# Kernel tuning notes

Measured on AMD Instinct MI355X. Metric: run time of the kernel, lower is better.

The kernel has to match this reference:

```python
import jax, jax.numpy as jnp
import numpy as np

D = 128
N_AUTHOR = 100000
N_PAPER = 200000
N_LAYERS = 2


def setup_inputs() -> dict:
    key = jax.random.key(0)
    ks = jax.random.split(key, 16)
    inp = {
        "x_author": jax.random.normal(ks[0], (N_AUTHOR, D), dtype=jnp.float32),
        "x_paper": jax.random.normal(ks[1], (N_PAPER, D), dtype=jnp.float32),
        "edge_index": jax.random.randint(ks[2], (2, 500000), 0, 100000, dtype=jnp.int32),
        "coauthor_edge_index": jax.random.randint(ks[3], (2, 250000), 0, 100000, dtype=jnp.int32),
        "supervision_edge_index": jax.random.randint(ks[4], (2, 100000), 0, 100000, dtype=jnp.int32),
    }
    scale = 1.0 / np.sqrt(D)
    names = ["W_a2p", "W_p2a", "W_aself", "W_pself", "W_co"]
    for i, n in enumerate(names):
        inp[n] = jax.random.uniform(ks[5 + i], (N_LAYERS, D, D), jnp.float32, -scale, scale)
        inp["b" + n[1:]] = jax.random.uniform(ks[10 + i], (N_LAYERS, D), jnp.float32, -scale, scale)
    return inp


def _linear(x, W, b):
    # torch.nn.Linear: y = x @ W.T + b
    return x @ W.T + b


def reference(x_author, x_paper, edge_index, coauthor_edge_index, supervision_edge_index,
              W_a2p, b_a2p, W_p2a, b_p2a, W_aself, b_aself, W_pself, b_pself, W_co, b_co):
    author_idx, paper_idx = edge_index[0], edge_index[1]
    co_src, co_dst = coauthor_edge_index[0], coauthor_edge_index[1]
    for l in range(N_LAYERS):
        # author -> paper messages
        msg_a = _linear(x_author[author_idx], W_a2p[l], b_a2p[l])       # [E, D]
        agg_to_papers = jax.ops.segment_sum(msg_a, paper_idx, num_segments=x_paper.shape[0])
        # paper -> author messages
        msg_p = _linear(x_paper[paper_idx], W_p2a[l], b_p2a[l])         # [E, D]
        agg_to_authors = jax.ops.segment_sum(msg_p, author_idx, num_segments=x_author.shape[0])
        x_paper = agg_to_papers + _linear(x_paper, W_pself[l], b_pself[l])
        x_author = agg_to_authors + _linear(x_author, W_aself[l], b_aself[l])
        # coauthor edges (author -> author)
        msg_co = _linear(x_author[co_src], W_co[l], b_co[l])            # [E_co, D]
        agg_co = jax.ops.segment_sum(msg_co, co_dst, num_segments=x_author.shape[0])
        x_author = x_author + agg_co
    a = x_author[supervision_edge_index[0]]
    p = x_paper[supervision_edge_index[1]]
    return (a * p).sum(axis=1)
```

## Files before the change

### kernel.cpp

```cpp
#include <hip/hip_runtime.h>

#define DD 128

typedef __attribute__((ext_vector_type(8))) short short8;
typedef __attribute__((ext_vector_type(4))) float f32x4;

__device__ inline unsigned short f2bf(float f) {
    unsigned u = __float_as_uint(f);
    unsigned r = (u + 0x7fffu + ((u >> 16) & 1u)) >> 16;
    return (unsigned short)r;
}
__device__ inline float bf2f(unsigned short u) {
    return __uint_as_float(((unsigned)u) << 16);
}
__device__ inline float bflo(unsigned u) { return __uint_as_float(u << 16); }
__device__ inline float bfhi(unsigned u) { return __uint_as_float(u & 0xffff0000u); }
__device__ inline unsigned pack2(float a, float b) {
    return (unsigned)f2bf(a) | ((unsigned)f2bf(b) << 16);
}

__global__ __launch_bounds__(256) void conv_all(const float* __restrict__ inA, unsigned short* __restrict__ outA, int n4A,
                                                const float* __restrict__ inP, unsigned short* __restrict__ outP, int n4P) {
    int i = blockIdx.x * blockDim.x + threadIdx.x;
    const float* in;
    unsigned short* out;
    int j;
    if (i < n4A) { in = inA; out = outA; j = i; }
    else if (i < n4A + n4P) { in = inP; out = outP; j = i - n4A; }
    else return;
    float4 v = *(const float4*)(in + (size_t)j * 4);
    uint2 o;
    o.x = pack2(v.x, v.y);
    o.y = pack2(v.z, v.w);
    *(uint2*)(out + (size_t)j * 4) = o;
}

__global__ __launch_bounds__(256) void pack_all(const float* __restrict__ Wa2p, const float* __restrict__ Wpself,
                                                const float* __restrict__ Wp2a, const float* __restrict__ Waself,
                                                const float* __restrict__ Wco,
                                                short* __restrict__ BPp0, short* __restrict__ BPp1,
                                                short* __restrict__ BPa0, short* __restrict__ BPa1,
                                                short* __restrict__ BPc0, short* __restrict__ BPc1) {
    const int WL = 128 * 128;
    int idx = blockIdx.x * blockDim.x + threadIdx.x;
    int seg = idx >> 12;
    int sidx = idx & 4095;
    const float *W1, *W2;
    short* dst;
    int ktiles;
    switch (seg) {
        case 0: W1 = Wa2p;      W2 = Wpself;      dst = BPp0; ktiles = 8; break;
        case 1: W1 = Wa2p + WL; W2 = Wpself + WL; dst = BPp1; ktiles = 8; break;
        case 2: W1 = Wp2a;      W2 = Waself;      dst = BPa0; ktiles = 8; break;
        case 3: W1 = Wp2a + WL; W2 = Waself + WL; dst = BPa1; ktiles = 8; break;
        case 4: W1 = Wco;       W2 = nullptr;     dst = BPc0; ktiles = 4; break;
        default: W1 = Wco + WL; W2 = nullptr;     dst = BPc1; ktiles = 4; break;
    }
    int total = 8 * ktiles * 64;
    if (sidx >= total) return;
    int lane = sidx & 63;
    int kk = (sidx >> 6) % ktiles;
    int t = (sidx >> 6) / ktiles;
    int n = t * 16 + (lane & 15);
    int kbase = kk * 32 + (lane >> 4) * 8;
    short8 v;
#pragma unroll
    for (int j = 0; j < 8; ++j) {
        int k = kbase + j;
        float f = (k < 128) ? W1[n * 128 + k] : W2[n * 128 + (k - 128)];
        v[j] = (short)f2bf(f);
    }
    *(short8*)(dst + (size_t)sidx * 8) = v;
}

__global__ __launch_bounds__(256) void count_all(const int* __restrict__ aidx, const int* __restrict__ pidx,
                                                 const int* __restrict__ cod,
                                                 int* __restrict__ cntP, int* __restrict__ cntA,
                                                 int* __restrict__ cntC, int E, int Eco) {
    int i = blockIdx.x * blockDim.x + threadIdx.x;
    if (i < E) {
        atomicAdd(&cntP[pidx[i]], 1);
        atomicAdd(&cntA[aidx[i]], 1);
    } else if (i < E + Eco) {
        atomicAdd(&cntC[cod[i - E]], 1);
    }
}

__global__ __launch_bounds__(256) void scan_local3(const int* __restrict__ c0, int* __restrict__ r0, int* __restrict__ p0, int N0,
                                                   const int* __restrict__ c1, int* __restrict__ r1, int* __restrict__ p1, int N1,
                                                   const int* __restrict__ c2, int* __restrict__ r2, int* __restrict__ p2, int N2,
                                                   int nb0, int nb1) {
    __shared__ int sh[256];
    int b = blockIdx.x;
    const int* cnt; int* row; int* partials; int N; int lb;
    if (b < nb0) { cnt = c0; row = r0; partials = p0; N = N0; lb = b; }
    else if (b < nb0 + nb1) { cnt = c1; row = r1; partials = p1; N = N1; lb = b - nb0; }
    else { cnt = c2; row = r2; partials = p2; N = N2; lb = b - nb0 - nb1; }
    int t = threadIdx.x;
    int base = lb * 1024 + t * 4;
    int v0 = 0, v1 = 0, v2 = 0, v3 = 0;
    if (base + 0 < N) v0 = cnt[base + 0];
    if (base + 1 < N) v1 = cnt[base + 1];
    if (base + 2 < N) v2 = cnt[base + 2];
    if (base + 3 < N) v3 = cnt[base + 3];
    sh[t] = v0 + v1 + v2 + v3;
    __syncthreads();
    for (int off = 1; off < 256; off <<= 1) {
        int y = (t >= off) ? sh[t - off] : 0;
        __syncthreads();
        sh[t] += y;
        __syncthreads();
    }
    int excl = (t > 0) ? sh[t - 1] : 0;
    if (t == 255) partials[lb] = sh[255];
    if (base + 0 < N) row[base + 0] = excl; excl += v0;
    if (base + 1 < N) row[base + 1] = excl; excl += v1;
    if (base + 2 < N) row[base + 2] = excl; excl += v2;
    if (base + 3 < N) row[base + 3] = excl;
}

__global__ __launch_bounds__(256) void scan_partials3(int* __restrict__ p0, int nb0,
                                                      int* __restrict__ p1, int nb1,
                                                      int* __restrict__ p2, int nb2) {
    __shared__ int sh[256];
    int* partials; int nb;
    if (blockIdx.x == 0) { partials = p0; nb = nb0; }
    else if (blockIdx.x == 1) { partials = p1; nb = nb1; }
    else { partials = p2; nb = nb2; }
    int t = threadIdx.x;
    int v = (t < nb) ? partials[t] : 0;
    sh[t] = v;
    __syncthreads();
    for (int off = 1; off < 256; off <<= 1) {
        int y = (t >= off) ? sh[t - off] : 0;
        __syncthreads();
        sh[t] += y;
        __syncthreads();
    }
    if (t < nb) partials[t] = (t > 0) ? sh[t - 1] : 0;
}

__global__ __launch_bounds__(256) void scan_finalize3(int* __restrict__ r0, int* __restrict__ cu0, const int* __restrict__ p0, int N0,
                                                      int* __restrict__ r1, int* __restrict__ cu1, const int* __restrict__ p1, int N1,
                                                      int* __restrict__ r2, int* __restrict__ cu2, const int* __restrict__ p2, int N2,
                                                      int fb0, int fb1) {
    int b = blockIdx.x;
    int* row; int* cur; const int* partials; int N; int lb;
    if (b < fb0) { row = r0; cur = cu0; partials = p0; N = N0; lb = b; }
    else if (b < fb0 + fb1) { row = r1; cur = cu1; partials = p1; N = N1; lb = b - fb0; }
    else { row = r2; cur = cu2; partials = p2; N = N2; lb = b - fb0 - fb1; }
    int i = lb * 256 + threadIdx.x;
    if (i >= N) return;
    int r = row[i] + partials[i >> 10];
    row[i] = r;
    cur[i] = r;
}

__global__ __launch_bounds__(256) void fill_all(const int* __restrict__ aidx, const int* __restrict__ pidx,
                                                const int* __restrict__ cos_, const int* __restrict__ cod,
                                                int* __restrict__ curP, int* __restrict__ curA, int* __restrict__ curC,
                                                int* __restrict__ adjP, int* __restrict__ adjA, int* __restrict__ adjC,
                                                int E, int Eco) {
    int i = blockIdx.x * blockDim.x + threadIdx.x;
    if (i < E) {
        int a = aidx[i], pp = pidx[i];
        adjP[atomicAdd(&curP[pp], 1)] = a;
        adjA[atomicAdd(&curA[a], 1)] = pp;
    } else if (i < E + Eco) {
        adjC[atomicAdd(&curC[cod[i - E]], 1)] = cos_[i - E];
    }
}

struct FParams {
    const unsigned short* gsrc;
    const unsigned short* selfx;
    const unsigned short* base;
    const int* adj;
    const int* rowp;
    const int* cnt;
    const short* Bpack;
    const float* b1;
    const float* b2;
    unsigned short* out;
    int M;
};

template <int KTILES, bool HAS_B2, bool ADD_BASE>
__device__ __forceinline__ void fused_body(char* lds, const FParams& p, int blk) {
    const int tid = threadIdx.x;
    const int node0 = blk * 64;
    const int grp = tid >> 4;
    const int l = tid & 15;

    int stA[4], dA[4];
#pragma unroll
    for (int i = 0; i < 4; ++i) {
        int node = node0 + grp * 4 + i;
        bool ok = node < p.M;
        stA[i] = ok ? p.rowp[node] : 0;
        dA[i] = ok ? p.cnt[node] : 0;
    }

    float acc[4][8];
#pragma unroll
    for (int i = 0; i < 4; ++i)
#pragma unroll
        for (int j = 0; j < 8; ++j) acc[i][j] = 0.f;

    int dmax = dA[0];
#pragma unroll
    for (int i = 1; i < 4; ++i) dmax = dA[i] > dmax ? dA[i] : dmax;

    for (int k = 0; k < dmax; k += 4) {
#pragma unroll
        for (int i = 0; i < 4; ++i) {
            if (k < dA[i]) {
                int st = stA[i] + k;
                int rem = dA[i] - k;
                int s0 = p.adj[st];
                int s1 = p.adj[st + ((rem > 1) ? 1 : 0)];
                int s2 = p.adj[st + ((rem > 2) ? 2 : 0)];
                int s3 = p.adj[st + ((rem > 3) ? 3 : 0)];
                float w1 = (rem > 1) ? 1.f : 0.f;
                float w2 = (rem > 2) ? 1.f : 0.f;
                float w3 = (rem > 3) ? 1.f : 0.f;
                uint4 v0 = *(const uint4*)(p.gsrc + (size_t)s0 * DD + l * 8);
                uint4 v1 = *(const uint4*)(p.gsrc + (size_t)s1 * DD + l * 8);
                uint4 v2 = *(const uint4*)(p.gsrc + (size_t)s2 * DD + l * 8);
                uint4 v3 = *(const uint4*)(p.gsrc + (size_t)s3 * DD + l * 8);
                acc[i][0] += bflo(v0.x); acc[i][1] += bfhi(v0.x);
                acc[i][2] += bflo(v0.y); acc[i][3] += bfhi(v0.y);
                acc[i][4] += bflo(v0.z); acc[i][5] += bfhi(v0.z);
                acc[i][6] += bflo(v0.w); acc[i][7] += bfhi(v0.w);
                acc[i][0] += w1 * bflo(v1.x); acc[i][1] += w1 * bfhi(v1.x);
                acc[i][2] += w1 * bflo(v1.y); acc[i][3] += w1 * bfhi(v1.y);
                acc[i][4] += w1 * bflo(v1.z); acc[i][5] += w1 * bfhi(v1.z);
                acc[i][6] += w1 * bflo(v1.w); acc[i][7] += w1 * bfhi(v1.w);
                acc[i][0] += w2 * bflo(v2.x); acc[i][1] += w2 * bfhi(v2.x);
                acc[i][2] += w2 * bflo(v2.y); acc[i][3] += w2 * bfhi(v2.y);
                acc[i][4] += w2 * bflo(v2.z); acc[i][5] += w2 * bfhi(v2.z);
                acc[i][6] += w2 * bflo(v2.w); acc[i][7] += w2 * bfhi(v2.w);
                acc[i][0] += w3 * bflo(v3.x); acc[i][1] += w3 * bfhi(v3.x);
                acc[i][2] += w3 * bflo(v3.y); acc[i][3] += w3 * bfhi(v3.y);
                acc[i][4] += w3 * bflo(v3.z); acc[i][5] += w3 * bfhi(v3.z);
                acc[i][6] += w3 * bflo(v3.w); acc[i][7] += w3 * bfhi(v3.w);
            }
        }
    }

#pragma unroll
    for (int i = 0; i < 4; ++i) {
        int lr = grp * 4 + i;
        uint4 o = make_uint4(pack2(acc[i][0], acc[i][1]), pack2(acc[i][2], acc[i][3]),
                             pack2(acc[i][4], acc[i][5]), pack2(acc[i][6], acc[i][7]));
        int colb = l * 16;
        *(uint4*)(lds + lr * 256 + (colb ^ ((lr & 7) << 4))) = o;
    }
    __syncthreads();

    const int wave = tid >> 6;
    const int lane = tid & 63;
    const int kg = lane >> 4;
    const int lrA = wave * 16 + (lane & 15);

    f32x4 facc[8];
#pragma unroll
    for (int t = 0; t < 8; ++t) facc[t] = (f32x4){0.f, 0.f, 0.f, 0.f};

#pragma unroll
    for (int kk = 0; kk < 4; ++kk) {
        int colb = kk * 64 + kg * 16;
        short8 af = *(const short8*)(lds + lrA * 256 + (colb ^ ((lrA & 7) << 4)));
#pragma unroll
        for (int t = 0; t < 8; ++t) {
            short8 bf = *(const short8*)(p.Bpack + ((size_t)(t * KTILES + kk) * 64 + lane) * 8);
            facc[t] = __builtin_amdgcn_mfma_f32_16x16x32_bf16(af, bf, facc[t], 0, 0, 0);
        }
    }
    if (KTILES == 8) {
        int srow = node0 + wave * 16 + (lane & 15);
        if (srow >= p.M) srow = p.M - 1;
        const unsigned short* sp = p.selfx + (size_t)srow * DD + kg * 8;
#pragma unroll
        for (int kk = 4; kk < 8; ++kk) {
            short8 af = *(const short8*)(sp + (kk - 4) * 32);
#pragma unroll
            for (int t = 0; t < 8; ++t) {
                short8 bf = *(const short8*)(p.Bpack + ((size_t)(t * 8 + kk) * 64 + lane) * 8);
                facc[t] = __builtin_amdgcn_mfma_f32_16x16x32_bf16(af, bf, facc[t], 0, 0, 0);
            }
        }
    }

    const int col0 = lane & 15;
    const int crow0 = node0 + wave * 16 + kg * 4;
#pragma unroll
    for (int t = 0; t < 8; ++t) {
        int col = t * 16 + col0;
        float bb = p.b1[col];
        float b2v = HAS_B2 ? p.b2[col] : 0.f;
#pragma unroll
        for (int r = 0; r < 4; ++r) {
            int row = crow0 + r;
            if (row < p.M) {
                float v = facc[t][r] + (float)p.cnt[row] * bb + b2v;
                if (ADD_BASE) v += bf2f(p.base[(size_t)row * DD + col]);
                p.out[(size_t)row * DD + col] = f2bf(v);
            }
        }
    }
}

__global__ __launch_bounds__(256, 5) void fused_dual_kernel(FParams pP, FParams pA, int blkP) {
    __shared__ char lds[16384];
    bool isP = (int)blockIdx.x < blkP;
    const FParams& p = isP ? pP : pA;
    fused_body<8, true, false>(lds, p, isP ? blockIdx.x : blockIdx.x - blkP);
}

__global__ __launch_bounds__(256, 5) void fused_co_kernel(FParams p) {
    __shared__ char lds[16384];
    fused_body<4, false, true>(lds, p, blockIdx.x);
}

__global__ __launch_bounds__(256) void dot_kernel(
    const unsigned short* __restrict__ xa, const unsigned short* __restrict__ xp,
    const int* __restrict__ s0, const int* __restrict__ s1,
    float* __restrict__ out, int E) {
    int g = blockIdx.x * blockDim.x + threadIdx.x;
    int e = g >> 4;
    int l = g & 15;
    if (e >= E) return;
    int a = s0[e], p = s1[e];
    uint4 va = *(const uint4*)(xa + (size_t)a * DD + l * 8);
    uint4 vp = *(const uint4*)(xp + (size_t)p * DD + l * 8);
    float s = bflo(va.x) * bflo(vp.x) + bfhi(va.x) * bfhi(vp.x)
            + bflo(va.y) * bflo(vp.y) + bfhi(va.y) * bfhi(vp.y)
            + bflo(va.z) * bflo(vp.z) + bfhi(va.z) * bfhi(vp.z)
            + bflo(va.w) * bflo(vp.w) + bfhi(va.w) * bfhi(vp.w);
    s += __shfl_xor(s, 1); s += __shfl_xor(s, 2);
    s += __shfl_xor(s, 4); s += __shfl_xor(s, 8);
    if (l == 0) out[e] = s;
}

extern "C" void kernel_launch(void* const* d_in, const int* in_sizes, int n_in,
                              void* d_out, int out_size, void* d_ws, size_t ws_size,
                              hipStream_t stream) {
    const float* xa_in = (const float*)d_in[0];
    const float* xp_in = (const float*)d_in[1];
    const int* eidx = (const int*)d_in[2];
    const int* co = (const int*)d_in[3];
    const int* sup = (const int*)d_in[4];
    const float* W_a2p = (const float*)d_in[5];
    const float* b_a2p = (const float*)d_in[6];
    const float* W_p2a = (const float*)d_in[7];
    const float* b_p2a = (const float*)d_in[8];
    const float* W_aself = (const float*)d_in[9];
    const float* b_aself = (const float*)d_in[10];
    const float* W_pself = (const float*)d_in[11];
    const float* b_pself = (const float*)d_in[12];
    const float* W_co = (const float*)d_in[13];
    const float* b_co = (const float*)d_in[14];

    const int NA = in_sizes[0] / DD;
    const int NP = in_sizes[1] / DD;
    const int E = in_sizes[2] / 2;
    const int Eco = in_sizes[3] / 2;
    const int Esup = in_sizes[4] / 2;
    const int* a_idx = eidx;
    const int* p_idx = eidx + E;
    const int* co_s = co;
    const int* co_d = co + Eco;
    const int* s0 = sup;
    const int* s1 = sup + Esup;

    char* w = (char*)d_ws;
    auto carve = [&](size_t bytes) -> char* {
        char* p = w;
        w += (bytes + 255) & ~(size_t)255;
        return p;
    };
    unsigned short* XA = (unsigned short*)carve((size_t)NA * DD * 2);
    unsigned short* XP = (unsigned short*)carve((size_t)NP * DD * 2);
    unsigned short* P0b = (unsigned short*)carve((size_t)NP * DD * 2);
    unsigned short* P1b = (unsigned short*)carve((size_t)NP * DD * 2);
    unsigned short* A0b = (unsigned short*)carve((size_t)NA * DD * 2);
    unsigned short* A1b = (unsigned short*)carve((size_t)NA * DD * 2);
    int* cntP = (int*)carve((size_t)NP * 4);
    int* rowP = (int*)carve((size_t)NP * 4);
    int* curP = (int*)carve((size_t)NP * 4);
    int* cntA = (int*)carve((size_t)NA * 4);
    int* rowA = (int*)carve((size_t)NA * 4);
    int* curA = (int*)carve((size_t)NA * 4);
    int* cntC = (int*)carve((size_t)NA * 4);
    int* rowC = (int*)carve((size_t)NA * 4);
    int* curC = (int*)carve((size_t)NA * 4);
    int* adjP = (int*)carve((size_t)E * 4);
    int* adjA = (int*)carve((size_t)E * 4);
    int* adjC = (int*)carve((size_t)Eco * 4);
    int* partP = (int*)carve(256 * 4);
    int* partA = (int*)carve(256 * 4);
    int* partC = (int*)carve(256 * 4);
    short* BPp0 = (short*)carve(8 * 8 * 64 * 8 * 2);
    short* BPp1 = (short*)carve(8 * 8 * 64 * 8 * 2);
    short* BPa0 = (short*)carve(8 * 8 * 64 * 8 * 2);
    short* BPa1 = (short*)carve(8 * 8 * 64 * 8 * 2);
    short* BPc0 = (short*)carve(8 * 4 * 64 * 8 * 2);
    short* BPc1 = (short*)carve(8 * 4 * 64 * 8 * 2);

    int n4A = NA * DD / 4, n4P = NP * DD / 4;
    conv_all<<<(n4A + n4P + 255) / 256, 256, 0, stream>>>(xa_in, XA, n4A, xp_in, XP, n4P);
    pack_all<<<96, 256, 0, stream>>>(W_a2p, W_pself, W_p2a, W_aself, W_co, BPp0, BPp1, BPa0, BPa1, BPc0, BPc1);

    hipMemsetAsync(cntP, 0, (size_t)NP * 4, stream);
    hipMemsetAsync(cntA, 0, (size_t)NA * 4, stream);
    hipMemsetAsync(cntC, 0, (size_t)NA * 4, stream);
    count_all<<<(E + Eco + 255) / 256, 256, 0, stream>>>(a_idx, p_idx, co_d, cntP, cntA, cntC, E, Eco);
    const int nbP = (NP + 1023) / 1024;
    const int nbA = (NA + 1023) / 1024;
    scan_local3<<<nbP + nbA + nbA, 256, 0, stream>>>(cntP, rowP, partP, NP, cntA, rowA, partA, NA, cntC, rowC, partC, NA, nbP, nbA);
    scan_partials3<<<3, 256, 0, stream>>>(partP, nbP, partA, nbA, partC, nbA);
    const int fbP = (NP + 255) / 256;
    const int fbA = (NA + 255) / 256;
    scan_finalize3<<<fbP + fbA + fbA, 256, 0, stream>>>(rowP, curP, partP, NP, rowA, curA, partA, NA, rowC, curC, partC, NA, fbP, fbA);
    fill_all<<<(E + Eco + 255) / 256, 256, 0, stream>>>(a_idx, p_idx, co_s, co_d, curP, curA, curC, adjP, adjA, adjC, E, Eco);

    const int blkP = (NP + 63) / 64;
    const int blkA = (NA + 63) / 64;

    FParams pP1 = {XA, XP, nullptr, adjP, rowP, cntP, BPp0, b_a2p, b_pself, P0b, NP};
    FParams pA1 = {XP, XA, nullptr, adjA, rowA, cntA, BPa0, b_p2a, b_aself, A0b, NA};
    FParams pC1 = {A0b, nullptr, A0b, adjC, rowC, cntC, BPc0, b_co, nullptr, A1b, NA};
    FParams pP2 = {A1b, P0b, nullptr, adjP, rowP, cntP, BPp1, b_a2p + 128, b_pself + 128, P1b, NP};
    FParams pA2 = {P0b, A1b, nullptr, adjA, rowA, cntA, BPa1, b_p2a + 128, b_aself + 128, A0b, NA};
    FParams pC2 = {A0b, nullptr, A0b, adjC, rowC, cntC, BPc1, b_co + 128, nullptr, A1b, NA};

    fused_dual_kernel<<<blkP + blkA, 256, 0, stream>>>(pP1, pA1, blkP);
    fused_co_kernel<<<blkA, 256, 0, stream>>>(pC1);
    fused_dual_kernel<<<blkP + blkA, 256, 0, stream>>>(pP2, pA2, blkP);
    fused_co_kernel<<<blkA, 256, 0, stream>>>(pC2);

    dot_kernel<<<(Esup * 16 + 255) / 256, 256, 0, stream>>>(A1b, P1b, s0, s1, (float*)d_out, Esup);
}
```

Baseline: 536.9 us.

## Stage block adjacency in LDS, halve gather unroll, raise occupancy, merge memsets

```diff
diff --git a/kernel.cpp b/kernel.cpp
--- a/kernel.cpp
+++ b/kernel.cpp
@@ -1,6 +1,7 @@
 #include <hip/hip_runtime.h>
 
 #define DD 128
+#define ADJ_CAP 1024
 
 typedef __attribute__((ext_vector_type(8))) short short8;
 typedef __attribute__((ext_vector_type(4))) float f32x4;
@@ -186,20 +187,27 @@
 };
 
 template <int KTILES, bool HAS_B2, bool ADD_BASE>
-__device__ __forceinline__ void fused_body(char* lds, const FParams& p, int blk) {
+__device__ __forceinline__ void fused_body(char* lds, int* ldsAdj, const FParams& p, int blk) {
     const int tid = threadIdx.x;
     const int node0 = blk * 64;
     const int grp = tid >> 4;
     const int l = tid & 15;
 
-    int stA[4], dA[4];
+    const int lastNode = (node0 + 63 < p.M) ? node0 + 63 : p.M - 1;
+    const int est = p.rowp[node0];
+    const int eend = p.rowp[lastNode] + p.cnt[lastNode];
+    const int nE = eend - est;
+    for (int j = tid; j < nE && j < ADJ_CAP; j += 256) ldsAdj[j] = p.adj[est + j];
+
+    int relSt[4], dA[4];
 #pragma unroll
     for (int i = 0; i < 4; ++i) {
         int node = node0 + grp * 4 + i;
         bool ok = node < p.M;
-        stA[i] = ok ? p.rowp[node] : 0;
+        relSt[i] = ok ? (p.rowp[node] - est) : 0;
         dA[i] = ok ? p.cnt[node] : 0;
     }
+    __syncthreads();
 
     float acc[4][8];
 #pragma unroll
@@ -211,23 +219,18 @@
 #pragma unroll
     for (int i = 1; i < 4; ++i) dmax = dA[i] > dmax ? dA[i] : dmax;
 
-    for (int k = 0; k < dmax; k += 4) {
+    for (int k = 0; k < dmax; k += 2) {
 #pragma unroll
         for (int i = 0; i < 4; ++i) {
             if (k < dA[i]) {
-                int st = stA[i] + k;
                 int rem = dA[i] - k;
-                int s0 = p.adj[st];
-                int s1 = p.adj[st + ((rem > 1) ? 1 : 0)];
-                int s2 = p.adj[st + ((rem > 2) ? 2 : 0)];
-                int s3 = p.adj[st + ((rem > 3) ? 3 : 0)];
+                int o0 = relSt[i] + k;
+                int o1 = o0 + ((rem > 1) ? 1 : 0);
+                int s0 = (o0 < ADJ_CAP) ? ldsAdj[o0] : p.adj[est + o0];
+                int s1 = (o1 < ADJ_CAP) ? ldsAdj[o1] : p.adj[est + o1];
                 float w1 = (rem > 1) ? 1.f : 0.f;
-                float w2 = (rem > 2) ? 1.f : 0.f;
-                float w3 = (rem > 3) ? 1.f : 0.f;
                 uint4 v0 = *(const uint4*)(p.gsrc + (size_t)s0 * DD + l * 8);
                 uint4 v1 = *(const uint4*)(p.gsrc + (size_t)s1 * DD + l * 8);
-                uint4 v2 = *(const uint4*)(p.gsrc + (size_t)s2 * DD + l * 8);
-                uint4 v3 = *(const uint4*)(p.gsrc + (size_t)s3 * DD + l * 8);
                 acc[i][0] += bflo(v0.x); acc[i][1] += bfhi(v0.x);
                 acc[i][2] += bflo(v0.y); acc[i][3] += bfhi(v0.y);
                 acc[i][4] += bflo(v0.z); acc[i][5] += bfhi(v0.z);
@@ -236,14 +239,6 @@
                 acc[i][2] += w1 * bflo(v1.y); acc[i][3] += w1 * bfhi(v1.y);
                 acc[i][4] += w1 * bflo(v1.z); acc[i][5] += w1 * bfhi(v1.z);
                 acc[i][6] += w1 * bflo(v1.w); acc[i][7] += w1 * bfhi(v1.w);
-                acc[i][0] += w2 * bflo(v2.x); acc[i][1] += w2 * bfhi(v2.x);
-                acc[i][2] += w2 * bflo(v2.y); acc[i][3] += w2 * bfhi(v2.y);
-                acc[i][4] += w2 * bflo(v2.z); acc[i][5] += w2 * bfhi(v2.z);
-                acc[i][6] += w2 * bflo(v2.w); acc[i][7] += w2 * bfhi(v2.w);
-                acc[i][0] += w3 * bflo(v3.x); acc[i][1] += w3 * bfhi(v3.x);
-                acc[i][2] += w3 * bflo(v3.y); acc[i][3] += w3 * bfhi(v3.y);
-                acc[i][4] += w3 * bflo(v3.z); acc[i][5] += w3 * bfhi(v3.z);
-                acc[i][6] += w3 * bflo(v3.w); acc[i][7] += w3 * bfhi(v3.w);
             }
         }
     }
@@ -311,16 +306,18 @@
     }
 }
 
-__global__ __launch_bounds__(256, 5) void fused_dual_kernel(FParams pP, FParams pA, int blkP) {
+__global__ __launch_bounds__(256, 8) void fused_dual_kernel(FParams pP, FParams pA, int blkP) {
     __shared__ char lds[16384];
+    __shared__ int ldsAdj[ADJ_CAP];
     bool isP = (int)blockIdx.x < blkP;
     const FParams& p = isP ? pP : pA;
-    fused_body<8, true, false>(lds, p, isP ? blockIdx.x : blockIdx.x - blkP);
-}
-
-__global__ __launch_bounds__(256, 5) void fused_co_kernel(FParams p) {
+    fused_body<8, true, false>(lds, ldsAdj, p, isP ? blockIdx.x : blockIdx.x - blkP);
+}
+
+__global__ __launch_bounds__(256, 8) void fused_co_kernel(FParams p) {
     __shared__ char lds[16384];
-    fused_body<4, false, true>(lds, p, blockIdx.x);
+    __shared__ int ldsAdj[ADJ_CAP];
+    fused_body<4, false, true>(lds, ldsAdj, p, blockIdx.x);
 }
 
 __global__ __launch_bounds__(256) void dot_kernel(
@@ -387,12 +384,13 @@
     unsigned short* A0b = (unsigned short*)carve((size_t)NA * DD * 2);
     unsigned short* A1b = (unsigned short*)carve((size_t)NA * DD * 2);
     int* cntP = (int*)carve((size_t)NP * 4);
+    int* cntA = (int*)carve((size_t)NA * 4);
+    int* cntC = (int*)carve((size_t)NA * 4);
+    size_t cntSpan = (size_t)((char*)cntC - (char*)cntP) + (((size_t)NA * 4 + 255) & ~(size_t)255);
     int* rowP = (int*)carve((size_t)NP * 4);
     int* curP = (int*)carve((size_t)NP * 4);
-    int* cntA = (int*)carve((size_t)NA * 4);
     int* rowA = (int*)carve((size_t)NA * 4);
     int* curA = (int*)carve((size_t)NA * 4);
-    int* cntC = (int*)carve((size_t)NA * 4);
     int* rowC = (int*)carve((size_t)NA * 4);
     int* curC = (int*)carve((size_t)NA * 4);
     int* adjP = (int*)carve((size_t)E * 4);
@@ -412,9 +410,7 @@
     conv_all<<<(n4A + n4P + 255) / 256, 256, 0, stream>>>(xa_in, XA, n4A, xp_in, XP, n4P);
     pack_all<<<96, 256, 0, stream>>>(W_a2p, W_pself, W_p2a, W_aself, W_co, BPp0, BPp1, BPa0, BPa1, BPc0, BPc1);
 
-    hipMemsetAsync(cntP, 0, (size_t)NP * 4, stream);
-    hipMemsetAsync(cntA, 0, (size_t)NA * 4, stream);
-    hipMemsetAsync(cntC, 0, (size_t)NA * 4, stream);
+    hipMemsetAsync(cntP, 0, cntSpan, stream);
     count_all<<<(E + Eco + 255) / 256, 256, 0, stream>>>(a_idx, p_idx, co_d, cntP, cntA, cntC, E, Eco);
     const int nbP = (NP + 1023) / 1024;
     const int nbA = (NA + 1023) / 1024;
```

After: 619.2 us. 1.15x slower.
